# Kernel tuning notes

Measured on AMD Instinct MI355X. Metric: run time of the kernel, lower is better.

Reference implementation:

```python
import jax, jax.numpy as jnp
import numpy as np

N = 50000   # nodes
E = 800000  # directed edges (self-loops added inside reference)
F_IN, H, C = 128, 96, 32


def setup_inputs() -> dict:
    key = jax.random.key(0)
    ks = jax.random.split(key, 8)
    x = jax.random.normal(ks[0], (N, F_IN), dtype=jnp.float32)
    edge_index = jax.random.randint(ks[1], (2, E), 0, N, dtype=jnp.int64)
    W1 = jax.random.normal(ks[2], (F_IN, H), dtype=jnp.float32) * 0.05
    b1 = jnp.zeros((H,), dtype=jnp.float32)
    W2 = jax.random.normal(ks[3], (H, H), dtype=jnp.float32) * 0.05
    b2 = jnp.zeros((H,), dtype=jnp.float32)
    W3 = jax.random.normal(ks[4], (H, C), dtype=jnp.float32) * 0.05
    b3 = jnp.zeros((C,), dtype=jnp.float32)
    return {"x": x, "edge_index": edge_index, "W1": W1, "b1": b1,
            "W2": W2, "b2": b2, "W3": W3, "b3": b3}


def gcn_conv(x, W, b, src, dst, n):
    """PyG GCNConv: x' = D^{-1/2} (A+I) D^{-1/2} (x W) + b (self-loops in src/dst)."""
    xw = x @ W                                        # [n, out]
    ones = jnp.ones(src.shape[0], dtype=xw.dtype)
    deg = jax.ops.segment_sum(ones, dst, num_segments=n)
    dinv = jnp.where(deg > 0, jax.lax.rsqrt(jnp.maximum(deg, 1.0)), 0.0)
    norm = dinv[src] * dinv[dst]                      # [E+n]
    msg = norm[:, None] * xw[src]                     # gather + scale
    out = jax.ops.segment_sum(msg, dst, num_segments=n)  # scatter-add
    return out + b


def reference(x, edge_index, W1, b1, W2, b2, W3, b3):
    loop = jnp.arange(N, dtype=edge_index.dtype)
    src = jnp.concatenate([edge_index[0], loop])      # add self-loops once
    dst = jnp.concatenate([edge_index[1], loop])
    h = jax.nn.relu(gcn_conv(x, W1, b1, src, dst, N))   # dropout is identity (eval)
    h = jax.nn.relu(gcn_conv(h, W2, b2, src, dst, N))
    h = gcn_conv(h, W3, b3, src, dst, N)
    return jax.nn.log_softmax(h, axis=1)
```

## Files before the change

### kernel.cpp

```cpp
#include <hip/hip_runtime.h>
#include <hip/hip_fp16.h>


typedef _Float16 half8 __attribute__((ext_vector_type(8)));
typedef float f32x4 __attribute__((ext_vector_type(4)));

constexpr int CAP = 64;
constexpr int NPB = 128;
constexpr int NBINS_P = 512;
constexpr int EPB = 4096;
constexpr int BCAP = 2560;

__device__ inline unsigned char f_to_fp8(float f) {
    f = fminf(fmaxf(f, -448.0f), 448.0f);
    unsigned short u = __half_as_ushort(__float2half(f * 0.00390625f));
    unsigned short mag = (unsigned short)((u & 0x7FFF) + 0x40);
    return (unsigned char)(((u >> 8) & 0x80) | (mag >> 7));
}

__device__ inline float2 fp8x2_to_f2_scaled(unsigned int w) {
    unsigned int lo = ((w << 7) & 0x3F80u) | ((w << 8) & 0x8000u);
    unsigned int hi = ((w >> 1) & 0x3F80u) | (w & 0x8000u);
    union { unsigned int u; __half2 h; } cv;
    cv.u = lo | (hi << 16);
    return __half22float2(cv.h);
}

__device__ inline float4 fp8x4_to_f4_scaled(unsigned int w) {
    float2 lo = fp8x2_to_f2_scaled(w & 0xFFFFu);
    float2 hi = fp8x2_to_f2_scaled(w >> 16);
    return {lo.x, lo.y, hi.x, hi.y};
}

__global__ __launch_bounds__(256) void prep_kernel(const int* __restrict__ ei, int twoE,
                                                   int* __restrict__ flags,
                                                   int* __restrict__ bin_cnt,
                                                   const float* __restrict__ W1,
                                                   const float* __restrict__ W2,
                                                   const float* __restrict__ W3,
                                                   __half* __restrict__ Wt1,
                                                   __half* __restrict__ Wt2,
                                                   __half* __restrict__ Wt3) {
    if (blockIdx.x == 0) {
        if (threadIdx.x < 8) flags[threadIdx.x] = 0;
        for (int b = threadIdx.x; b < NBINS_P; b += 256) bin_cnt[b] = 0;
        __syncthreads();
        int c = 0;
        for (int j = threadIdx.x; j < 2048 && j < twoE; j += 256) {
            if ((j & 1) && ei[j] != 0) c++;
        }
        if (c) atomicAdd(&flags[4], c);
        return;
    }
    int i = (blockIdx.x - 1) * 256 + threadIdx.x;
    if (i < 128 * 96) {
        int f = i / 128, k = i - f * 128;
        Wt1[i] = __float2half(W1[(size_t)k * 96 + f]);
    } else if (i < 128 * 96 + 96 * 96) {
        int j = i - 128 * 96;
        int f = j / 96, k = j - f * 96;
        Wt2[j] = __float2half(W2[(size_t)k * 96 + f]);
    } else if (i < 128 * 96 + 96 * 96 + 96 * 32) {
        int j = i - 128 * 96 - 96 * 96;
        int f = j / 96, k = j - f * 96;
        Wt3[j] = __float2half(W3[(size_t)k * 32 + f]);
    }
}

__device__ inline int ld_idx(const int* ei, int half_, int i, int E, bool i64) {
    return i64 ? ei[2 * (half_ * (size_t)E + i)] : ei[half_ * (size_t)E + i];
}

__global__ __launch_bounds__(256) void part_kernel(const int* __restrict__ ei,
                                                   const int* __restrict__ flags,
                                                   int* __restrict__ bin_cnt,
                                                   int* __restrict__ bins, int E, int n) {
    __shared__ int hist[NBINS_P], excl[NBINS_P], cur[NBINS_P], gpos[NBINS_P];
    __shared__ int tmp[256];
    __shared__ int stage[EPB];
    const int tid = threadIdx.x;
    const bool i64 = (flags[4] == 0);
    for (int b = tid; b < NBINS_P; b += 256) hist[b] = 0;
    __syncthreads();

    int v[EPB / 256];
    const int base = blockIdx.x * EPB;
#pragma unroll
    for (int j = 0; j < EPB / 256; j++) {
        int i = base + j * 256 + tid;
        v[j] = -1;
        if (i < E) {
            int s = ld_idx(ei, 0, i, E, i64);
            int d = ld_idx(ei, 1, i, E, i64);
            if ((unsigned)s < (unsigned)n && (unsigned)d < (unsigned)n) {
                int bin = d >> 7, ln = d & 127;
                v[j] = (bin << 23) | (ln << 16) | s;
                atomicAdd(&hist[bin], 1);
            }
        }
    }
    __syncthreads();
    int a0 = hist[2 * tid], a1 = hist[2 * tid + 1];
    int pairsum = a0 + a1;
    tmp[tid] = pairsum;
    __syncthreads();
    for (int off = 1; off < 256; off <<= 1) {
        int t = (tid >= off) ? tmp[tid - off] : 0;
        __syncthreads();
        tmp[tid] += t;
        __syncthreads();
    }
    int S = tmp[tid] - pairsum;
    excl[2 * tid] = S;
    excl[2 * tid + 1] = S + a0;
    cur[2 * tid] = S;
    cur[2 * tid + 1] = S + a0;
    __syncthreads();
    for (int b = tid; b < NBINS_P; b += 256)
        gpos[b] = hist[b] ? atomicAdd(&bin_cnt[b], hist[b]) : 0;
#pragma unroll
    for (int j = 0; j < EPB / 256; j++) {
        if (v[j] != -1) {
            int bin = ((unsigned)v[j]) >> 23;
            int p = atomicAdd(&cur[bin], 1);
            stage[p] = v[j];
        }
    }
    __syncthreads();
    int total = excl[NBINS_P - 1] + hist[NBINS_P - 1];
    for (int i = tid; i < total; i += 256) {
        int w = stage[i];
        int bin = ((unsigned)w) >> 23;
        int k = gpos[bin] + (i - excl[bin]);
        if (k < BCAP) bins[(size_t)bin * BCAP + k] = w;
    }
}

__global__ __launch_bounds__(256) void build_kernel(const int* __restrict__ bin_cnt,
                                                    const int* __restrict__ bins,
                                                    int* __restrict__ cnt,
                                                    unsigned short* __restrict__ csr, int n) {
    __shared__ unsigned short lcsr[NPB * CAP];
    __shared__ int lcnt[NPB];
    const int b = blockIdx.x, tid = threadIdx.x;
    for (int i = tid; i < NPB; i += 256) lcnt[i] = 0;
    __syncthreads();
    int m = min(bin_cnt[b], BCAP);
    for (int i = tid; i < m; i += 256) {
        int w = bins[(size_t)b * BCAP + i];
        int ln = (w >> 16) & 127;
        int p = atomicAdd(&lcnt[ln], 1);
        if (p < CAP) lcsr[ln * CAP + p] = (unsigned short)(w & 0xFFFF);
    }
    __syncthreads();
    const int node0 = b * NPB;
    const unsigned int* l32 = (const unsigned int*)lcsr;
    unsigned int* c32 = (unsigned int*)(csr + (size_t)node0 * CAP);
    for (int i = tid; i < NPB * CAP / 2; i += 256) {
        int node = node0 + (i >> 5);
        if (node < n) c32[i] = l32[i];
    }
    for (int t = tid; t < NPB; t += 256)
        if (node0 + t < n) cnt[node0 + t] = lcnt[t];
}

__device__ inline half8 to_h8(float4 u0, float4 u1) {
    half8 r;
    r[0] = (_Float16)u0.x; r[1] = (_Float16)u0.y; r[2] = (_Float16)u0.z; r[3] = (_Float16)u0.w;
    r[4] = (_Float16)u1.x; r[5] = (_Float16)u1.y; r[6] = (_Float16)u1.z; r[7] = (_Float16)u1.w;
    return r;
}

template <int K, int F, bool XF32, bool OUT8>
__global__ __launch_bounds__(256) void gemm_mfma(const void* __restrict__ X,
                                                 const __half* __restrict__ Wt,
                                                 const int* __restrict__ cnt,
                                                 void* __restrict__ out, int n) {
    constexpr int KP = K + 8;
    constexpr int FT = F / 16;
    constexpr int KC = K / 32;
    __shared__ _Float16 Wl[F * KP];
    for (int i = threadIdx.x; i < F * (K / 8); i += 256) {
        int f = i / (K / 8), c = i - f * (K / 8);
        *(half8*)&Wl[f * KP + c * 8] = *(const half8*)&Wt[(size_t)f * K + c * 8];
    }
    __syncthreads();
    const int wave = threadIdx.x >> 6, lane = threadIdx.x & 63;
    const int node0 = (blockIdx.x * 4 + wave) * 16;
    if (node0 >= n) return;
    const int m = lane & 15, q = lane >> 4;
    const int arow = min(node0 + m, n - 1);

    half8 af[KC];
    if (XF32) {
        const float* xp = (const float*)X + (size_t)arow * K + q * 8;
#pragma unroll
        for (int kc = 0; kc < KC; kc++) {
            float4 u0 = *(const float4*)(xp + kc * 32);
            float4 u1 = *(const float4*)(xp + kc * 32 + 4);
            af[kc] = to_h8(u0, u1);
        }
    } else {
        const __half* xp = (const __half*)X + (size_t)arow * K + q * 8;
#pragma unroll
        for (int kc = 0; kc < KC; kc++) af[kc] = *(const half8*)(xp + kc * 32);
    }

    f32x4 acc[FT];
#pragma unroll
    for (int t = 0; t < FT; t++) acc[t] = (f32x4)0.f;
#pragma unroll
    for (int kc = 0; kc < KC; kc++) {
#pragma unroll
        for (int t = 0; t < FT; t++) {
            half8 b = *(const half8*)&Wl[(t * 16 + m) * KP + kc * 32 + q * 8];
            acc[t] = __builtin_amdgcn_mfma_f32_16x16x32_f16(af[kc], b, acc[t], 0, 0, 0);
        }
    }
    float dv[4];
#pragma unroll
    for (int r = 0; r < 4; r++) {
        int node = node0 + q * 4 + r;
        dv[r] = (node < n) ? rsqrtf(1.0f + (float)cnt[node]) : 0.f;
    }
#pragma unroll
    for (int t = 0; t < FT; t++)
#pragma unroll
        for (int r = 0; r < 4; r++) {
            int node = node0 + q * 4 + r;
            if (node < n) {
                float vv = acc[t][r] * dv[r];
                if (OUT8)
                    ((unsigned char*)out)[(size_t)node * F + t * 16 + m] = f_to_fp8(vv);
                else
                    ((__half*)out)[(size_t)node * F + t * 16 + m] = __float2half(vv);
            }
        }
}

__global__ __launch_bounds__(256) void agg96_fp8(const unsigned char* __restrict__ xws,
                                                 const int* __restrict__ cnt,
                                                 const unsigned short* __restrict__ csr,
                                                 const float* __restrict__ bias,
                                                 __half* __restrict__ out, int n) {
    int node = blockIdx.x * 4 + (threadIdx.x >> 6);
    int lane = threadIdx.x & 63;
    if (node >= n) return;
    const int g = lane < 24 ? 0 : 1;
    const int c = g ? lane - 24 : lane;
    const bool act = lane < 48;
    int deg = cnt[node];
    int m = min(deg, CAP);
    float dvs = rsqrtf(1.0f + (float)deg) * 256.0f;
    const unsigned short* row = csr + (size_t)node * CAP;
    float4 a = {0.f, 0.f, 0.f, 0.f};
    if (lane < 24) {
        unsigned int w = *(const unsigned int*)(xws + (size_t)node * 96 + c * 4);
        a = fp8x4_to_f4_scaled(w);
    }
    int e = 0;
    for (; e + 8 <= m; e += 8) {
        uint4 pr = *(const uint4*)&row[e];
        if (act) {
            unsigned int w[4];
            int u0 = g ? (pr.x >> 16) : (pr.x & 0xFFFF);
            int u1 = g ? (pr.y >> 16) : (pr.y & 0xFFFF);
            int u2 = g ? (pr.z >> 16) : (pr.z & 0xFFFF);
            int u3 = g ? (pr.w >> 16) : (pr.w & 0xFFFF);
            w[0] = *(const unsigned int*)(xws + (size_t)u0 * 96 + c * 4);
            w[1] = *(const unsigned int*)(xws + (size_t)u1 * 96 + c * 4);
            w[2] = *(const unsigned int*)(xws + (size_t)u2 * 96 + c * 4);
            w[3] = *(const unsigned int*)(xws + (size_t)u3 * 96 + c * 4);
#pragma unroll
            for (int j = 0; j < 4; j++) {
                float4 f = fp8x4_to_f4_scaled(w[j]);
                a.x += f.x; a.y += f.y; a.z += f.z; a.w += f.w;
            }
        }
    }
    for (; e + 2 <= m; e += 2) {
        unsigned int pr = *(const unsigned int*)&row[e];
        if (act) {
            int u = g ? (pr >> 16) : (pr & 0xFFFF);
            unsigned int w = *(const unsigned int*)(xws + (size_t)u * 96 + c * 4);
            float4 f = fp8x4_to_f4_scaled(w);
            a.x += f.x; a.y += f.y; a.z += f.z; a.w += f.w;
        }
    }
    if (e < m && lane < 24) {
        int u = row[e];
        unsigned int w = *(const unsigned int*)(xws + (size_t)u * 96 + c * 4);
        float4 f = fp8x4_to_f4_scaled(w);
        a.x += f.x; a.y += f.y; a.z += f.z; a.w += f.w;
    }
    float px = __shfl(a.x, lane + 24);
    float py = __shfl(a.y, lane + 24);
    float pz = __shfl(a.z, lane + 24);
    float pw = __shfl(a.w, lane + 24);
    if (lane < 24) {
        a.x += px; a.y += py; a.z += pz; a.w += pw;
        float4 bb = *(const float4*)&bias[c * 4];
        float r0 = fmaxf(fmaf(dvs, a.x, bb.x), 0.f);
        float r1 = fmaxf(fmaf(dvs, a.y, bb.y), 0.f);
        float r2 = fmaxf(fmaf(dvs, a.z, bb.z), 0.f);
        float r3 = fmaxf(fmaf(dvs, a.w, bb.w), 0.f);
        union { __half2 h[2]; uint2 u; } pk;
        pk.h[0] = __floats2half2_rn(r0, r1);
        pk.h[1] = __floats2half2_rn(r2, r3);
        *(uint2*)(out + (size_t)node * 96 + c * 4) = pk.u;
    }
}

__global__ __launch_bounds__(256) void agg32_lsm(const __half* __restrict__ xws,
                                                 const int* __restrict__ cnt,
                                                 const unsigned short* __restrict__ csr,
                                                 const float* __restrict__ bias,
                                                 float* __restrict__ out, int n) {
    int node = blockIdx.x * 4 + (threadIdx.x >> 6);
    int lane = threadIdx.x & 63;
    if (node >= n) return;
    const int g = lane >> 4, l = lane & 15;
    int deg = cnt[node];
    int m = min(deg, CAP);
    float dv = rsqrtf(1.0f + (float)deg);
    const unsigned short* row = csr + (size_t)node * CAP;
    float2 a = {0.f, 0.f};
    if (g == 0) a = __half22float2(*(const __half2*)(xws + (size_t)node * 32 + l * 2));
    int e = 0;
    for (; e + 4 <= m; e += 4) {
        uint2 pr = *(const uint2*)&row[e];
        unsigned int h = (g & 2) ? pr.y : pr.x;
        int u = (g & 1) ? (int)(h >> 16) : (int)(h & 0xFFFF);
        float2 f = __half22float2(*(const __half2*)(xws + (size_t)u * 32 + l * 2));
        a.x += f.x; a.y += f.y;
    }
    for (; e < m; e++) {
        if (g == 0) {
            int u = row[e];
            float2 f = __half22float2(*(const __half2*)(xws + (size_t)u * 32 + l * 2));
            a.x += f.x; a.y += f.y;
        }
    }
    a.x += __shfl_xor(a.x, 16); a.y += __shfl_xor(a.y, 16);
    a.x += __shfl_xor(a.x, 32); a.y += __shfl_xor(a.y, 32);
    if (g == 0) {
        float2 b = *(const float2*)&bias[l * 2];
        float rx = fmaf(dv, a.x, b.x), ry = fmaf(dv, a.y, b.y);
        float mx = fmaxf(rx, ry);
        mx = fmaxf(mx, __shfl_xor(mx, 1));
        mx = fmaxf(mx, __shfl_xor(mx, 2));
        mx = fmaxf(mx, __shfl_xor(mx, 4));
        mx = fmaxf(mx, __shfl_xor(mx, 8));
        float s = expf(rx - mx) + expf(ry - mx);
        s += __shfl_xor(s, 1);
        s += __shfl_xor(s, 2);
        s += __shfl_xor(s, 4);
        s += __shfl_xor(s, 8);
        float ls = logf(s);
        ((float2*)out)[(size_t)node * 16 + l] = {rx - mx - ls, ry - mx - ls};
    }
}

extern "C" void kernel_launch(void* const* d_in, const int* in_sizes, int n_in,
                              void* d_out, int out_size, void* d_ws, size_t ws_size,
                              hipStream_t stream) {
    const float* x  = (const float*)d_in[0];
    const int*   ei = (const int*)d_in[1];
    const float* W1 = (const float*)d_in[2];
    const float* b1 = (const float*)d_in[3];
    const float* W2 = (const float*)d_in[4];
    const float* b2 = (const float*)d_in[5];
    const float* W3 = (const float*)d_in[6];
    const float* b3 = (const float*)d_in[7];
    float* out = (float*)d_out;

    const int N_ = in_sizes[0] / 128;
    const int E_ = in_sizes[1] / 2;
    const int NBINS = (N_ + NPB - 1) / NPB;

    char* base = (char*)d_ws;
    size_t off = 0;
    auto take = [&](size_t bytes) {
        void* p = base + off;
        off = (off + bytes + 255) & ~(size_t)255;
        return p;
    };
    int*    flags   = (int*)take(4 * 8);
    int*    bin_cnt = (int*)take(4 * NBINS_P);
    int*    bins    = (int*)take(4 * (size_t)NBINS * BCAP);
    int*    cnt     = (int*)take(4 * (size_t)N_);
    unsigned short* csr = (unsigned short*)take(2 * (size_t)N_ * CAP);
    __half* Wt1     = (__half*)take(2 * 128 * 96);
    __half* Wt2     = (__half*)take(2 * 96 * 96);
    __half* Wt3     = (__half*)take(2 * 96 * 32);
    unsigned char* bufA = (unsigned char*)take(2 * (size_t)N_ * 96);
    __half* bufB    = (__half*)take(2 * (size_t)N_ * 96);

    const int prepBlocks = 1 + (128 * 96 + 96 * 96 + 96 * 32 + 255) / 256;
    prep_kernel<<<prepBlocks, 256, 0, stream>>>(ei, in_sizes[1], flags, bin_cnt,
                                                W1, W2, W3, Wt1, Wt2, Wt3);
    part_kernel<<<(E_ + EPB - 1) / EPB, 256, 0, stream>>>(ei, flags, bin_cnt, bins, E_, N_);
    build_kernel<<<NBINS, 256, 0, stream>>>(bin_cnt, bins, cnt, csr, N_);

    const int gGemm = (N_ + 63) / 64;
    const int gAgg  = (N_ + 3) / 4;

    gemm_mfma<128, 96, true, true><<<gGemm, 256, 0, stream>>>(x, Wt1, cnt, bufA, N_);
    agg96_fp8<<<gAgg, 256, 0, stream>>>(bufA, cnt, csr, b1, bufB, N_);
    gemm_mfma<96, 96, false, true><<<gGemm, 256, 0, stream>>>(bufB, Wt2, cnt, bufA, N_);
    agg96_fp8<<<gAgg, 256, 0, stream>>>(bufA, cnt, csr, b2, bufB, N_);
    gemm_mfma<96, 32, false, false><<<gGemm, 256, 0, stream>>>(bufB, Wt3, cnt, bufA, N_);
    agg32_lsm<<<gAgg, 256, 0, stream>>>((const __half*)bufA, cnt, csr, b3, out, N_);
}
```

Before: 234.3 us.

## Drop prep kernel, use per-tile bin slots, widen aggregation index loads

Result: slower. 244.9 us (+4.5%).

```diff
diff --git a/kernel.cpp b/kernel.cpp
--- a/kernel.cpp
+++ b/kernel.cpp
@@ -9,7 +9,7 @@
 constexpr int NPB = 128;
 constexpr int NBINS_P = 512;
 constexpr int EPB = 4096;
-constexpr int BCAP = 2560;
+constexpr int TCAP = 40;
 
 __device__ inline unsigned char f_to_fp8(float f) {
     f = fminf(fmaxf(f, -448.0f), 448.0f);
@@ -32,59 +32,55 @@
     return {lo.x, lo.y, hi.x, hi.y};
 }
 
-__global__ __launch_bounds__(256) void prep_kernel(const int* __restrict__ ei, int twoE,
-                                                   int* __restrict__ flags,
-                                                   int* __restrict__ bin_cnt,
+__device__ inline int ld_idx(const int* ei, int half_, int i, int E, bool i64) {
+    return i64 ? ei[2 * (half_ * (size_t)E + i)] : ei[half_ * (size_t)E + i];
+}
+
+__global__ __launch_bounds__(256) void part_kernel(const int* __restrict__ ei,
+                                                   int* __restrict__ tcnt,
+                                                   int* __restrict__ bins,
                                                    const float* __restrict__ W1,
                                                    const float* __restrict__ W2,
                                                    const float* __restrict__ W3,
                                                    __half* __restrict__ Wt1,
                                                    __half* __restrict__ Wt2,
-                                                   __half* __restrict__ Wt3) {
-    if (blockIdx.x == 0) {
-        if (threadIdx.x < 8) flags[threadIdx.x] = 0;
-        for (int b = threadIdx.x; b < NBINS_P; b += 256) bin_cnt[b] = 0;
-        __syncthreads();
-        int c = 0;
-        for (int j = threadIdx.x; j < 2048 && j < twoE; j += 256) {
-            if ((j & 1) && ei[j] != 0) c++;
-        }
-        if (c) atomicAdd(&flags[4], c);
-        return;
-    }
-    int i = (blockIdx.x - 1) * 256 + threadIdx.x;
-    if (i < 128 * 96) {
-        int f = i / 128, k = i - f * 128;
-        Wt1[i] = __float2half(W1[(size_t)k * 96 + f]);
-    } else if (i < 128 * 96 + 96 * 96) {
-        int j = i - 128 * 96;
-        int f = j / 96, k = j - f * 96;
-        Wt2[j] = __float2half(W2[(size_t)k * 96 + f]);
-    } else if (i < 128 * 96 + 96 * 96 + 96 * 32) {
-        int j = i - 128 * 96 - 96 * 96;
-        int f = j / 96, k = j - f * 96;
-        Wt3[j] = __float2half(W3[(size_t)k * 32 + f]);
-    }
-}
-
-__device__ inline int ld_idx(const int* ei, int half_, int i, int E, bool i64) {
-    return i64 ? ei[2 * (half_ * (size_t)E + i)] : ei[half_ * (size_t)E + i];
-}
-
-__global__ __launch_bounds__(256) void part_kernel(const int* __restrict__ ei,
-                                                   const int* __restrict__ flags,
-                                                   int* __restrict__ bin_cnt,
-                                                   int* __restrict__ bins, int E, int n) {
-    __shared__ int hist[NBINS_P], excl[NBINS_P], cur[NBINS_P], gpos[NBINS_P];
+                                                   __half* __restrict__ Wt3,
+                                                   int E, int n, int NT) {
+    __shared__ int hist[NBINS_P], excl[NBINS_P], cur[NBINS_P];
     __shared__ int tmp[256];
     __shared__ int stage[EPB];
+    __shared__ int i64flag;
     const int tid = threadIdx.x;
-    const bool i64 = (flags[4] == 0);
+    const int bid = blockIdx.x;
+
+    {
+        int i = bid * 256 + tid;
+        if (i < 128 * 96) {
+            int f = i / 128, k = i - f * 128;
+            Wt1[i] = __float2half(W1[(size_t)k * 96 + f]);
+        } else if (i < 128 * 96 + 96 * 96) {
+            int j = i - 128 * 96;
+            int f = j / 96, k = j - f * 96;
+            Wt2[j] = __float2half(W2[(size_t)k * 96 + f]);
+        } else if (i < 128 * 96 + 96 * 96 + 96 * 32) {
+            int j = i - 128 * 96 - 96 * 96;
+            int f = j / 96, k = j - f * 96;
+            Wt3[j] = __float2half(W3[(size_t)k * 32 + f]);
+        }
+    }
+    if (tid == 0) i64flag = 0;
     for (int b = tid; b < NBINS_P; b += 256) hist[b] = 0;
     __syncthreads();
+    int cdet = 0;
+    int twoE = 2 * E;
+    for (int j = 2 * tid + 1; j < 2048 && j < twoE; j += 512)
+        if (ei[j] != 0) cdet = 1;
+    if (cdet) atomicAdd(&i64flag, 1);
+    __syncthreads();
+    const bool i64 = (i64flag == 0);
 
     int v[EPB / 256];
-    const int base = blockIdx.x * EPB;
+    const int base = bid * EPB;
 #pragma unroll
     for (int j = 0; j < EPB / 256; j++) {
         int i = base + j * 256 + tid;
@@ -116,8 +112,7 @@
     cur[2 * tid] = S;
     cur[2 * tid + 1] = S + a0;
     __syncthreads();
-    for (int b = tid; b < NBINS_P; b += 256)
-        gpos[b] = hist[b] ? atomicAdd(&bin_cnt[b], hist[b]) : 0;
+    for (int b = tid; b < NBINS_P; b += 256) tcnt[bid * NBINS_P + b] = hist[b];
 #pragma unroll
     for (int j = 0; j < EPB / 256; j++) {
         if (v[j] != -1) {
@@ -131,26 +126,30 @@
     for (int i = tid; i < total; i += 256) {
         int w = stage[i];
         int bin = ((unsigned)w) >> 23;
-        int k = gpos[bin] + (i - excl[bin]);
-        if (k < BCAP) bins[(size_t)bin * BCAP + k] = w;
-    }
-}
-
-__global__ __launch_bounds__(256) void build_kernel(const int* __restrict__ bin_cnt,
+        int k = i - excl[bin];
+        if (k < TCAP) bins[((size_t)bin * NT + bid) * TCAP + k] = w;
+    }
+}
+
+__global__ __launch_bounds__(256) void build_kernel(const int* __restrict__ tcnt,
                                                     const int* __restrict__ bins,
                                                     int* __restrict__ cnt,
-                                                    unsigned short* __restrict__ csr, int n) {
+                                                    unsigned short* __restrict__ csr,
+                                                    int n, int NT) {
     __shared__ unsigned short lcsr[NPB * CAP];
     __shared__ int lcnt[NPB];
     const int b = blockIdx.x, tid = threadIdx.x;
+    const int g = tid >> 6, lane = tid & 63;
     for (int i = tid; i < NPB; i += 256) lcnt[i] = 0;
     __syncthreads();
-    int m = min(bin_cnt[b], BCAP);
-    for (int i = tid; i < m; i += 256) {
-        int w = bins[(size_t)b * BCAP + i];
-        int ln = (w >> 16) & 127;
-        int p = atomicAdd(&lcnt[ln], 1);
-        if (p < CAP) lcsr[ln * CAP + p] = (unsigned short)(w & 0xFFFF);
+    for (int t = g; t < NT; t += 4) {
+        int mt = min(tcnt[t * NBINS_P + b], TCAP);
+        if (lane < mt) {
+            int w = bins[((size_t)b * NT + t) * TCAP + lane];
+            int ln = (w >> 16) & 127;
+            int p = atomicAdd(&lcnt[ln], 1);
+            if (p < CAP) lcsr[ln * CAP + p] = (unsigned short)(w & 0xFFFF);
+        }
     }
     __syncthreads();
     const int node0 = b * NPB;
@@ -252,47 +251,73 @@
     int deg = cnt[node];
     int m = min(deg, CAP);
     float dvs = rsqrtf(1.0f + (float)deg) * 256.0f;
-    const unsigned short* row = csr + (size_t)node * CAP;
+    const uint4* r4 = (const uint4*)(csr + (size_t)node * CAP);
     float4 a = {0.f, 0.f, 0.f, 0.f};
     if (lane < 24) {
         unsigned int w = *(const unsigned int*)(xws + (size_t)node * 96 + c * 4);
         a = fp8x4_to_f4_scaled(w);
     }
     int e = 0;
-    for (; e + 8 <= m; e += 8) {
-        uint4 pr = *(const uint4*)&row[e];
+#define G96_U(pr_) (g ? ((pr_) >> 16) : ((pr_) & 0xFFFF))
+#define G96_LD(u_) (*(const unsigned int*)(xws + (size_t)(u_) * 96 + c * 4))
+    for (; e + 16 <= m; e += 16) {
+        uint4 pa = r4[e >> 3], pb = r4[(e >> 3) + 1];
         if (act) {
-            unsigned int w[4];
-            int u0 = g ? (pr.x >> 16) : (pr.x & 0xFFFF);
-            int u1 = g ? (pr.y >> 16) : (pr.y & 0xFFFF);
-            int u2 = g ? (pr.z >> 16) : (pr.z & 0xFFFF);
-            int u3 = g ? (pr.w >> 16) : (pr.w & 0xFFFF);
-            w[0] = *(const unsigned int*)(xws + (size_t)u0 * 96 + c * 4);
-            w[1] = *(const unsigned int*)(xws + (size_t)u1 * 96 + c * 4);
-            w[2] = *(const unsigned int*)(xws + (size_t)u2 * 96 + c * 4);
-            w[3] = *(const unsigned int*)(xws + (size_t)u3 * 96 + c * 4);
-#pragma unroll
-            for (int j = 0; j < 4; j++) {
-                float4 f = fp8x4_to_f4_scaled(w[j]);
-                a.x += f.x; a.y += f.y; a.z += f.z; a.w += f.w;
-            }
-        }
-    }
-    for (; e + 2 <= m; e += 2) {
-        unsigned int pr = *(const unsigned int*)&row[e];
+            unsigned int w0 = G96_LD(G96_U(pa.x)), w1 = G96_LD(G96_U(pa.y));
+            unsigned int w2 = G96_LD(G96_U(pa.z)), w3 = G96_LD(G96_U(pa.w));
+            unsigned int w4 = G96_LD(G96_U(pb.x)), w5 = G96_LD(G96_U(pb.y));
+            unsigned int w6 = G96_LD(G96_U(pb.z)), w7 = G96_LD(G96_U(pb.w));
+            float4 f;
+            f = fp8x4_to_f4_scaled(w0); a.x += f.x; a.y += f.y; a.z += f.z; a.w += f.w;
+            f = fp8x4_to_f4_scaled(w1); a.x += f.x; a.y += f.y; a.z += f.z; a.w += f.w;
+            f = fp8x4_to_f4_scaled(w2); a.x += f.x; a.y += f.y; a.z += f.z; a.w += f.w;
+            f = fp8x4_to_f4_scaled(w3); a.x += f.x; a.y += f.y; a.z += f.z; a.w += f.w;
+            f = fp8x4_to_f4_scaled(w4); a.x += f.x; a.y += f.y; a.z += f.z; a.w += f.w;
+            f = fp8x4_to_f4_scaled(w5); a.x += f.x; a.y += f.y; a.z += f.z; a.w += f.w;
+            f = fp8x4_to_f4_scaled(w6); a.x += f.x; a.y += f.y; a.z += f.z; a.w += f.w;
+            f = fp8x4_to_f4_scaled(w7); a.x += f.x; a.y += f.y; a.z += f.z; a.w += f.w;
+        }
+    }
+    if (e + 8 <= m) {
+        uint4 pa = r4[e >> 3];
         if (act) {
-            int u = g ? (pr >> 16) : (pr & 0xFFFF);
-            unsigned int w = *(const unsigned int*)(xws + (size_t)u * 96 + c * 4);
-            float4 f = fp8x4_to_f4_scaled(w);
+            unsigned int w0 = G96_LD(G96_U(pa.x)), w1 = G96_LD(G96_U(pa.y));
+            unsigned int w2 = G96_LD(G96_U(pa.z)), w3 = G96_LD(G96_U(pa.w));
+            float4 f;
+            f = fp8x4_to_f4_scaled(w0); a.x += f.x; a.y += f.y; a.z += f.z; a.w += f.w;
+            f = fp8x4_to_f4_scaled(w1); a.x += f.x; a.y += f.y; a.z += f.z; a.w += f.w;
+            f = fp8x4_to_f4_scaled(w2); a.x += f.x; a.y += f.y; a.z += f.z; a.w += f.w;
+            f = fp8x4_to_f4_scaled(w3); a.x += f.x; a.y += f.y; a.z += f.z; a.w += f.w;
+        }
+        e += 8;
+    }
+    if (e + 4 <= m) {
+        const unsigned int* r2 = (const unsigned int*)r4;
+        unsigned int p0 = r2[e >> 1], p1 = r2[(e >> 1) + 1];
+        if (act) {
+            unsigned int w0 = G96_LD(G96_U(p0)), w1 = G96_LD(G96_U(p1));
+            float4 f;
+            f = fp8x4_to_f4_scaled(w0); a.x += f.x; a.y += f.y; a.z += f.z; a.w += f.w;
+            f = fp8x4_to_f4_scaled(w1); a.x += f.x; a.y += f.y; a.z += f.z; a.w += f.w;
+        }
+        e += 4;
+    }
+    if (e + 2 <= m) {
+        unsigned int p0 = ((const unsigned int*)r4)[e >> 1];
+        if (act) {
+            unsigned int w0 = G96_LD(G96_U(p0));
+            float4 f = fp8x4_to_f4_scaled(w0);
             a.x += f.x; a.y += f.y; a.z += f.z; a.w += f.w;
         }
+        e += 2;
     }
     if (e < m && lane < 24) {
-        int u = row[e];
-        unsigned int w = *(const unsigned int*)(xws + (size_t)u * 96 + c * 4);
-        float4 f = fp8x4_to_f4_scaled(w);
+        int u = ((const unsigned short*)r4)[e];
+        float4 f = fp8x4_to_f4_scaled(G96_LD(u));
         a.x += f.x; a.y += f.y; a.z += f.z; a.w += f.w;
     }
+#undef G96_U
+#undef G96_LD
     float px = __shfl(a.x, lane + 24);
     float py = __shfl(a.y, lane + 24);
     float pz = __shfl(a.z, lane + 24);
@@ -323,24 +348,53 @@
     int deg = cnt[node];
     int m = min(deg, CAP);
     float dv = rsqrtf(1.0f + (float)deg);
-    const unsigned short* row = csr + (size_t)node * CAP;
+    const uint4* r4 = (const uint4*)(csr + (size_t)node * CAP);
     float2 a = {0.f, 0.f};
     if (g == 0) a = __half22float2(*(const __half2*)(xws + (size_t)node * 32 + l * 2));
+#define G32_U(pr_, j_) ((j_ & 1) ? (int)((j_ & 2 ? pr_.z : pr_.x) >> 16) \
+                                 : (int)((j_ & 2 ? pr_.z : pr_.x) & 0xFFFF))
+    auto ext = [](uint4 p, int j) -> int {
+        unsigned int h = (j & 4) ? ((j & 2) ? p.w : p.z) : ((j & 2) ? p.y : p.x);
+        return (j & 1) ? (int)(h >> 16) : (int)(h & 0xFFFF);
+    };
     int e = 0;
-    for (; e + 4 <= m; e += 4) {
-        uint2 pr = *(const uint2*)&row[e];
-        unsigned int h = (g & 2) ? pr.y : pr.x;
+    for (; e + 16 <= m; e += 16) {
+        uint4 pa = r4[e >> 3], pb = r4[(e >> 3) + 1];
+        int u0 = ext(pa, g), u1 = ext(pa, g + 4);
+        int u2 = ext(pb, g), u3 = ext(pb, g + 4);
+        float2 f0 = __half22float2(*(const __half2*)(xws + (size_t)u0 * 32 + l * 2));
+        float2 f1 = __half22float2(*(const __half2*)(xws + (size_t)u1 * 32 + l * 2));
+        float2 f2 = __half22float2(*(const __half2*)(xws + (size_t)u2 * 32 + l * 2));
+        float2 f3 = __half22float2(*(const __half2*)(xws + (size_t)u3 * 32 + l * 2));
+        a.x += f0.x + f1.x + f2.x + f3.x;
+        a.y += f0.y + f1.y + f2.y + f3.y;
+    }
+    if (e + 8 <= m) {
+        uint4 pa = r4[e >> 3];
+        int u0 = ext(pa, g), u1 = ext(pa, g + 4);
+        float2 f0 = __half22float2(*(const __half2*)(xws + (size_t)u0 * 32 + l * 2));
+        float2 f1 = __half22float2(*(const __half2*)(xws + (size_t)u1 * 32 + l * 2));
+        a.x += f0.x + f1.x;
+        a.y += f0.y + f1.y;
+        e += 8;
+    }
+    if (e + 4 <= m) {
+        unsigned int p0 = ((const unsigned int*)r4)[e >> 1];
+        unsigned int p1 = ((const unsigned int*)r4)[(e >> 1) + 1];
+        unsigned int h = (g & 2) ? p1 : p0;
         int u = (g & 1) ? (int)(h >> 16) : (int)(h & 0xFFFF);
         float2 f = __half22float2(*(const __half2*)(xws + (size_t)u * 32 + l * 2));
         a.x += f.x; a.y += f.y;
+        e += 4;
     }
     for (; e < m; e++) {
         if (g == 0) {
-            int u = row[e];
+            int u = ((const unsigned short*)r4)[e];
             float2 f = __half22float2(*(const __half2*)(xws + (size_t)u * 32 + l * 2));
             a.x += f.x; a.y += f.y;
         }
     }
+#undef G32_U
     a.x += __shfl_xor(a.x, 16); a.y += __shfl_xor(a.y, 16);
     a.x += __shfl_xor(a.x, 32); a.y += __shfl_xor(a.y, 32);
     if (g == 0) {
@@ -377,6 +431,7 @@
     const int N_ = in_sizes[0] / 128;
     const int E_ = in_sizes[1] / 2;
     const int NBINS = (N_ + NPB - 1) / NPB;
+    const int NT = (E_ + EPB - 1) / EPB;
 
     char* base = (char*)d_ws;
     size_t off = 0;
@@ -385,22 +440,19 @@
         off = (off + bytes + 255) & ~(size_t)255;
         return p;
     };
-    int*    flags   = (int*)take(4 * 8);
-    int*    bin_cnt = (int*)take(4 * NBINS_P);
-    int*    bins    = (int*)take(4 * (size_t)NBINS * BCAP);
-    int*    cnt     = (int*)take(4 * (size_t)N_);
+    int*    tcnt = (int*)take(4 * (size_t)NT * NBINS_P);
+    int*    bins = (int*)take(4 * (size_t)NBINS * NT * TCAP);
+    int*    cnt  = (int*)take(4 * (size_t)N_);
     unsigned short* csr = (unsigned short*)take(2 * (size_t)N_ * CAP);
-    __half* Wt1     = (__half*)take(2 * 128 * 96);
-    __half* Wt2     = (__half*)take(2 * 96 * 96);
-    __half* Wt3     = (__half*)take(2 * 96 * 32);
+    __half* Wt1  = (__half*)take(2 * 128 * 96);
+    __half* Wt2  = (__half*)take(2 * 96 * 96);
+    __half* Wt3  = (__half*)take(2 * 96 * 32);
     unsigned char* bufA = (unsigned char*)take(2 * (size_t)N_ * 96);
-    __half* bufB    = (__half*)take(2 * (size_t)N_ * 96);
-
-    const int prepBlocks = 1 + (128 * 96 + 96 * 96 + 96 * 32 + 255) / 256;
-    prep_kernel<<<prepBlocks, 256, 0, stream>>>(ei, in_sizes[1], flags, bin_cnt,
-                                                W1, W2, W3, Wt1, Wt2, Wt3);
-    part_kernel<<<(E_ + EPB - 1) / EPB, 256, 0, stream>>>(ei, flags, bin_cnt, bins, E_, N_);
-    build_kernel<<<NBINS, 256, 0, stream>>>(bin_cnt, bins, cnt, csr, N_);
+    __half* bufB = (__half*)take(2 * (size_t)N_ * 96);
+
+    part_kernel<<<NT, 256, 0, stream>>>(ei, tcnt, bins, W1, W2, W3, Wt1, Wt2, Wt3,
+                                        E_, N_, NT);
+    build_kernel<<<NBINS, 256, 0, stream>>>(tcnt, bins, cnt, csr, N_, NT);
 
     const int gGemm = (N_ + 63) / 64;
     const int gAgg  = (N_ + 3) / 4;
```
